# Performance work log

Hardware: AMD Instinct MI355X
Metric: run time of the kernel (lower is better)

## Reference

```python
import jax, jax.numpy as jnp
import numpy as np

B, S, D, H = 2, 2048, 1024, 16
DK = D // H


def setup_inputs() -> dict:
    key = jax.random.key(0)
    ks = jax.random.split(key, 8)
    Q = jax.random.normal(ks[0], (B, S, D), dtype=jnp.float32)
    K = jax.random.normal(ks[1], (B, S, D), dtype=jnp.float32)
    V = jax.random.normal(ks[2], (B, S, D), dtype=jnp.float32)
    scale = 0.02
    W_q = jax.random.normal(ks[3], (D, D), dtype=jnp.float32) * scale
    W_k = jax.random.normal(ks[4], (D, D), dtype=jnp.float32) * scale
    W_v = jax.random.normal(ks[5], (D, D), dtype=jnp.float32) * scale
    W_o = jax.random.normal(ks[6], (D, D), dtype=jnp.float32) * scale
    b_q = jnp.zeros((D,), jnp.float32)
    b_k = jnp.zeros((D,), jnp.float32)
    b_v = jnp.zeros((D,), jnp.float32)
    b_o = jnp.zeros((D,), jnp.float32)
    # causal mask, broadcastable [1,1,S,S]; mask==0 positions are masked out
    mask = jnp.tril(jnp.ones((S, S), jnp.int32))[None, None, :, :]
    return dict(Q=Q, K=K, V=V, W_q=W_q, b_q=b_q, W_k=W_k, b_k=b_k,
                W_v=W_v, b_v=b_v, W_o=W_o, b_o=b_o, mask=mask)


def reference(Q, K, V, W_q, b_q, W_k, b_k, W_v, b_v, W_o, b_o, mask):
    # linear projections (torch Linear equivalent up to weight layout)
    q = Q @ W_q + b_q   # [B,S,D]
    k = K @ W_k + b_k
    v = V @ W_v + b_v
    # split heads -> [B,H,S,DK]
    q = q.reshape(B, S, H, DK).transpose(0, 2, 1, 3)
    k = k.reshape(B, S, H, DK).transpose(0, 2, 1, 3)
    v = v.reshape(B, S, H, DK).transpose(0, 2, 1, 3)
    # scaled dot-product attention with explicit [B,H,S,S] scores
    scores = jnp.einsum('bhqd,bhkd->bhqk', q, k) / jnp.sqrt(jnp.float32(DK))
    scores = jnp.where(mask == 0, jnp.float32(-1e9), scores)
    attn = jax.nn.softmax(scores, axis=-1)
    out = jnp.einsum('bhqk,bhkd->bhqd', attn, v)
    # merge heads and output projection
    out = out.transpose(0, 2, 1, 3).reshape(B, S, D)
    return out @ W_o + b_o
```

## Files before the change

kernel.cpp:

```cpp
#include <hip/hip_runtime.h>


typedef unsigned short u16;
typedef __attribute__((ext_vector_type(8))) short s8v;
typedef __attribute__((ext_vector_type(4))) float f4v;

#define S_ 2048
#define D_ 1024
#define H_ 16
#define DK_ 64

__device__ __forceinline__ u16 f2bf(float f) {
  unsigned u = __builtin_bit_cast(unsigned, f);
  u += 0x7fffu + ((u >> 16) & 1u);
  return (u16)(u >> 16);
}
__device__ __forceinline__ u16 f2bf_t(float f) {
  return (u16)(__builtin_bit_cast(unsigned, f) >> 16);
}

__device__ __forceinline__ void gld_lds16(const u16* g, u16* l) {
  __builtin_amdgcn_global_load_lds(
      (const __attribute__((address_space(1))) unsigned int*)g,
      (__attribute__((address_space(3))) unsigned int*)l, 16, 0, 0);
}

__global__ __launch_bounds__(256) void prep(
    const float* __restrict__ Q, const float* __restrict__ K, const float* __restrict__ V,
    u16* __restrict__ Qc, u16* __restrict__ Kc, u16* __restrict__ Vc,
    const float* __restrict__ W0, const float* __restrict__ W1,
    const float* __restrict__ W2, const float* __restrict__ W3,
    u16* __restrict__ T0, u16* __restrict__ T1, u16* __restrict__ T2, u16* __restrict__ T3) {
  int bid = blockIdx.x, tid = threadIdx.x;
  if (bid < 3072) {
    int z = bid >> 10, t = bid & 1023;
    const float* s = z == 0 ? Q : z == 1 ? K : V;
    u16*         d = z == 0 ? Qc : z == 1 ? Kc : Vc;
    const int n4 = (2 * S_ * D_) / 4;
    for (int idx = t * 256 + tid; idx < n4; idx += 1024 * 256) {
      float4 f = ((const float4*)s)[idx];
      unsigned lo = (unsigned)f2bf(f.x) | ((unsigned)f2bf(f.y) << 16);
      unsigned hi = (unsigned)f2bf(f.z) | ((unsigned)f2bf(f.w) << 16);
      ((uint2*)d)[idx] = make_uint2(lo, hi);
    }
  } else {
    int wb = bid - 3072;
    int z = wb >> 10, t = wb & 1023;
    const float* W = z == 0 ? W0 : z == 1 ? W1 : z == 2 ? W2 : W3;
    u16*         T = z == 0 ? T0 : z == 1 ? T1 : z == 2 ? T2 : T3;
    __shared__ float tile[32][33];
    int tx = tid & 31, ty = tid >> 5;
    int c0 = (t & 31) * 32, r0 = (t >> 5) * 32;
#pragma unroll
    for (int i = 0; i < 32; i += 8)
      tile[ty + i][tx] = W[(size_t)(r0 + ty + i) * D_ + c0 + tx];
    __syncthreads();
#pragma unroll
    for (int i = 0; i < 32; i += 8)
      T[(size_t)(c0 + ty + i) * D_ + r0 + tx] = f2bf(tile[tx][ty + i]);
  }
}

#define BK_ 64

template <int MI, int NJ, int MODE>
__device__ __forceinline__ void gemm_core(const u16* __restrict__ A, const u16* __restrict__ Bt,
                                          const float* __restrict__ bias, void* __restrict__ out,
                                          float oscale, u16* lds) {
  constexpr int BM = MI * 32;
  constexpr int BN = NJ * 32;
  u16* Al = lds;
  u16* Bl = lds + BM * BK_;
  int tid = threadIdx.x;
  int w = tid >> 6, lane = tid & 63, quad = lane >> 4, col = lane & 15;
  int wm = (w >> 1) * (MI * 16), wn = (w & 1) * (NJ * 16);
  int m0 = blockIdx.y * BM, n0 = blockIdx.x * BN;
  f4v acc[MI][NJ] = {};
  const u16* Ag = A + (size_t)m0 * 1024;
  const u16* Bg = Bt + (size_t)n0 * 1024;
  int sr = tid >> 3, ss = tid & 7;

  for (int k0 = 0; k0 < 1024; k0 += BK_) {
    __syncthreads();
#pragma unroll
    for (int c = 0; c < BM / 32; ++c) {
      int r = c * 32 + sr;
      int gs = ss ^ (r & 7);
      gld_lds16(Ag + (size_t)r * 1024 + k0 + gs * 8, &Al[r * BK_ + ss * 8]);
    }
#pragma unroll
    for (int c = 0; c < BN / 32; ++c) {
      int r = c * 32 + sr;
      int gs = ss ^ (r & 7);
      gld_lds16(Bg + (size_t)r * 1024 + k0 + gs * 8, &Bl[r * BK_ + ss * 8]);
    }
    __syncthreads();
#pragma unroll
    for (int hf = 0; hf < 2; ++hf) {
      s8v af[MI], bfr[NJ];
#pragma unroll
      for (int i = 0; i < MI; ++i) {
        int row = wm + i * 16 + col;
        int sl = (hf * 4 + quad) ^ (row & 7);
        af[i] = *(const s8v*)&Al[row * BK_ + sl * 8];
      }
#pragma unroll
      for (int j = 0; j < NJ; ++j) {
        int row = wn + j * 16 + col;
        int sl = (hf * 4 + quad) ^ (row & 7);
        bfr[j] = *(const s8v*)&Bl[row * BK_ + sl * 8];
      }
#pragma unroll
      for (int i = 0; i < MI; ++i)
#pragma unroll
        for (int j = 0; j < NJ; ++j)
          acc[i][j] = __builtin_amdgcn_mfma_f32_16x16x32_bf16(af[i], bfr[j], acc[i][j], 0, 0, 0);
    }
  }

  if (MODE == 1) {
    __syncthreads();
    u16* scr = lds + w * 2304;
    int h = (n0 + wn) >> 6;
    int dkl = lane & 31, sh = (lane >> 5) * 32;
    int mg0 = m0 + wm + sh;
    int bb = mg0 >> 11, s0g = mg0 & 2047;
    u16* ob = (u16*)out + ((size_t)(bb * H_ + h) * DK_) * S_;
#pragma unroll
    for (int t = 0; t < 2; ++t) {
#pragma unroll
      for (int j2 = 2 * t; j2 < 2 * t + 2; ++j2) {
        float bv = bias[n0 + wn + j2 * 16 + col];
        int rloc = j2 * 16 + col - t * 32;
#pragma unroll
        for (int i = 0; i < MI; ++i)
#pragma unroll
          for (int r = 0; r < 4; ++r)
            scr[rloc * 72 + i * 16 + quad * 4 + r] = f2bf(acc[i][j2][r] + bv);
      }
      __builtin_amdgcn_wave_barrier();
      u16* op = ob + (size_t)(t * 32 + dkl) * S_ + s0g;
#pragma unroll
      for (int c = 0; c < 4; ++c)
        *(uint4*)&op[c * 8] = *(const uint4*)&scr[dkl * 72 + sh + c * 8];
      __builtin_amdgcn_wave_barrier();
    }
    return;
  }

#pragma unroll
  for (int i = 0; i < MI; ++i) {
#pragma unroll
    for (int j = 0; j < NJ; ++j) {
      int n = n0 + wn + j * 16 + col;
      float bb = bias[n];
#pragma unroll
      for (int r = 0; r < 4; ++r) {
        int m = m0 + wm + i * 16 + quad * 4 + r;
        float v = (acc[i][j][r] + bb) * oscale;
        if (MODE == 2) {
          ((float*)out)[(size_t)m * 1024 + n] = v;
        } else {
          int b = m >> 11, s = m & 2047, h = n >> 6, dk = n & 63;
          ((u16*)out)[((size_t)(b * H_ + h) * S_ + s) * DK_ + dk] = f2bf(v);
        }
      }
    }
  }
}

#define CEXPQ 0.18033688f

__global__ __launch_bounds__(256) void gemm_qkv(
    const u16* __restrict__ A0, const u16* __restrict__ A1, const u16* __restrict__ A2,
    const u16* __restrict__ B0, const u16* __restrict__ B1, const u16* __restrict__ B2,
    const float* __restrict__ bi0, const float* __restrict__ bi1, const float* __restrict__ bi2,
    u16* __restrict__ o0, u16* __restrict__ o1, u16* __restrict__ o2) {
  __shared__ __attribute__((aligned(16))) u16 lds[128 * BK_ + 128 * BK_];
  int z = blockIdx.z;
  const u16* A = z == 0 ? A0 : z == 1 ? A1 : A2;
  const u16* Bt = z == 0 ? B0 : z == 1 ? B1 : B2;
  const float* bias = z == 0 ? bi0 : z == 1 ? bi1 : bi2;
  u16* o = z == 0 ? o0 : z == 1 ? o1 : o2;
  if (z == 2)
    gemm_core<4, 4, 1>(A, Bt, bias, o, 1.0f, lds);
  else
    gemm_core<4, 4, 0>(A, Bt, bias, o, z == 0 ? CEXPQ : 1.0f, lds);
}

__global__ __launch_bounds__(256, 4) void gemm_out(const u16* __restrict__ A, const u16* __restrict__ Bt,
                                                   const float* __restrict__ bias, float* __restrict__ out) {
  __shared__ __attribute__((aligned(16))) u16 lds[64 * BK_ + 64 * BK_];
  gemm_core<2, 2, 2>(A, Bt, bias, out, 1.0f, lds);
}

#define KT_ 64
#define PSTR 72

__global__ __launch_bounds__(512, 4) void attn_fused(const u16* __restrict__ qb, const u16* __restrict__ kb,
                                                     const u16* __restrict__ vtb, u16* __restrict__ ao) {
  __shared__ __attribute__((aligned(16))) u16 Kt[KT_ * PSTR];
  __shared__ __attribute__((aligned(16))) u16 Vts[DK_ * PSTR];
  __shared__ __attribute__((aligned(16))) u16 Pl[8][16 * PSTR];
  int bh = blockIdx.y, b = bh >> 4, h = bh & 15;
  int j = blockIdx.x;
  int tid = threadIdx.x, w = tid >> 6, lane = tid & 63, quad = lane >> 4, col = lane & 15;
  int sub = w & 3;
  int base = (w < 4) ? (31 - j) * 64 : j * 64;
  int qmin = base + sub * 16;
  int nk = (32 - j) * 64;

  const u16* Qh = qb + (size_t)bh * S_ * DK_;
  const u16* Kh = kb + (size_t)bh * S_ * DK_;
  const u16* Vh = vtb + (size_t)bh * DK_ * S_;

  s8v qf0 = *(const s8v*)(Qh + (size_t)(qmin + col) * DK_ + quad * 8);
  s8v qf1 = *(const s8v*)(Qh + (size_t)(qmin + col) * DK_ + 32 + quad * 8);

  f4v O[4] = {};
  float ls[4] = {};

  int st = tid & 255;
  bool stK = tid < 256;
  int srow = st >> 2, soff = (st & 3) * 16;
  u16* sl = stK ? &Kt[srow * PSTR + soff] : &Vts[srow * PSTR + soff];
  const u16* g0 = stK ? Kh + (size_t)srow * DK_ + soff : Vh + (size_t)srow * S_ + soff;
  uint4 preA = *(const uint4*)g0;
  uint4 preB = *(const uint4*)(g0 + 8);

  for (int kt = 0; kt < nk; kt += KT_) {
    __syncthreads();
    *(uint4*)sl = preA;
    *(uint4*)(sl + 8) = preB;
    __syncthreads();
    int kn = kt + KT_;
    if (kn < nk) {
      const u16* gn = stK ? Kh + (size_t)(kn + srow) * DK_ + soff
                          : Vh + (size_t)srow * S_ + kn + soff;
      preA = *(const uint4*)gn;
      preB = *(const uint4*)(gn + 8);
    }
    if (kt > qmin + 15) continue;

    f4v sc[4];
#pragma unroll
    for (int ks = 0; ks < 4; ++ks) {
      s8v kf0 = *(const s8v*)&Kt[(ks * 16 + col) * PSTR + quad * 8];
      s8v kf1 = *(const s8v*)&Kt[(ks * 16 + col) * PSTR + 32 + quad * 8];
      f4v t = {0.f, 0.f, 0.f, 0.f};
      t = __builtin_amdgcn_mfma_f32_16x16x32_bf16(qf0, kf0, t, 0, 0, 0);
      t = __builtin_amdgcn_mfma_f32_16x16x32_bf16(qf1, kf1, t, 0, 0, 0);
      sc[ks] = t;
    }

    bool full = (kt + KT_ - 1 <= qmin);
#pragma unroll
    for (int r = 0; r < 4; ++r) {
      float p0, p1, p2, p3;
      if (full) {
        p0 = exp2f(sc[0][r]);
        p1 = exp2f(sc[1][r]);
        p2 = exp2f(sc[2][r]);
        p3 = exp2f(sc[3][r]);
      } else {
        int qr = qmin + quad * 4 + r;
        p0 = (kt + col)      <= qr ? exp2f(sc[0][r]) : 0.f;
        p1 = (kt + 16 + col) <= qr ? exp2f(sc[1][r]) : 0.f;
        p2 = (kt + 32 + col) <= qr ? exp2f(sc[2][r]) : 0.f;
        p3 = (kt + 48 + col) <= qr ? exp2f(sc[3][r]) : 0.f;
      }
      ls[r] += (p0 + p1) + (p2 + p3);
      int row = quad * 4 + r;
      Pl[w][row * PSTR + col]      = f2bf_t(p0);
      Pl[w][row * PSTR + 16 + col] = f2bf_t(p1);
      Pl[w][row * PSTR + 32 + col] = f2bf_t(p2);
      Pl[w][row * PSTR + 48 + col] = f2bf_t(p3);
    }
    __builtin_amdgcn_wave_barrier();

    s8v pa0 = *(const s8v*)&Pl[w][col * PSTR + quad * 8];
    s8v pa1 = *(const s8v*)&Pl[w][col * PSTR + 32 + quad * 8];
#pragma unroll
    for (int d = 0; d < 4; ++d) {
      s8v vf0 = *(const s8v*)&Vts[(d * 16 + col) * PSTR + quad * 8];
      s8v vf1 = *(const s8v*)&Vts[(d * 16 + col) * PSTR + 32 + quad * 8];
      O[d] = __builtin_amdgcn_mfma_f32_16x16x32_bf16(pa0, vf0, O[d], 0, 0, 0);
      O[d] = __builtin_amdgcn_mfma_f32_16x16x32_bf16(pa1, vf1, O[d], 0, 0, 0);
    }
    __builtin_amdgcn_wave_barrier();
  }

#pragma unroll
  for (int r = 0; r < 4; ++r) {
    float l = ls[r];
    l += __shfl_xor(l, 1);
    l += __shfl_xor(l, 2);
    l += __shfl_xor(l, 4);
    l += __shfl_xor(l, 8);
    float inv = 1.0f / l;
    size_t row = (size_t)(b * S_ + qmin + quad * 4 + r);
#pragma unroll
    for (int d = 0; d < 4; ++d)
      ao[row * D_ + h * DK_ + d * 16 + col] = f2bf(O[d][r] * inv);
  }
}

extern "C" void kernel_launch(void* const* d_in, const int* in_sizes, int n_in,
                              void* d_out, int out_size, void* d_ws, size_t ws_size,
                              hipStream_t stream) {
  const float* Q  = (const float*)d_in[0];
  const float* K  = (const float*)d_in[1];
  const float* V  = (const float*)d_in[2];
  const float* Wq = (const float*)d_in[3];
  const float* bq = (const float*)d_in[4];
  const float* Wk = (const float*)d_in[5];
  const float* bk = (const float*)d_in[6];
  const float* Wv = (const float*)d_in[7];
  const float* bv = (const float*)d_in[8];
  const float* Wo = (const float*)d_in[9];
  const float* bo = (const float*)d_in[10];

  char* p = (char*)d_ws;
  const size_t TEN = (size_t)2 * S_ * D_ * 2;
  const size_t WT  = (size_t)D_ * D_ * 2;
  u16* Qc  = (u16*)p; p += TEN;
  u16* Kc  = (u16*)p; p += TEN;
  u16* Vc  = (u16*)p; p += TEN;
  u16* Wqt = (u16*)p; p += WT;
  u16* Wkt = (u16*)p; p += WT;
  u16* Wvt = (u16*)p; p += WT;
  u16* Wot = (u16*)p; p += WT;
  u16* qb  = (u16*)p; p += TEN;
  u16* kbf = (u16*)p; p += TEN;
  u16* vtb = (u16*)p; p += TEN;
  u16* ao  = (u16*)p; p += TEN;

  prep<<<7168, 256, 0, stream>>>(Q, K, V, Qc, Kc, Vc, Wq, Wk, Wv, Wo, Wqt, Wkt, Wvt, Wot);
  gemm_qkv<<<dim3(D_ / 128, 32, 3), 256, 0, stream>>>(Qc, Kc, Vc, Wqt, Wkt, Wvt, bq, bk, bv, qb, kbf, vtb);
  attn_fused<<<dim3(16, 2 * H_), 512, 0, stream>>>(qb, kbf, vtb, ao);
  gemm_out<<<dim3(D_ / 64, 64), 256, 0, stream>>>(ao, Wot, bo, (float*)d_out);
}
```

Before: 235.7 us.

## Split attention key range across two blocks and combine partial results

Each attention block now handles only every other 64-key tile (interleaved by a half index), doubling the grid to 1024 blocks. The two blocks write unnormalized bf16 partial outputs and row sums, and a new combine kernel adds them, normalizes, and writes the merged-head layout. This aims to raise occupancy and parallelism on a grid that previously had only 512 blocks. In exchange it adds an extra kernel launch, extra global traffic for the partials, and bf16 rounding of the unnormalized partials. It appears to rely on a fixed softmax offset (no running max), so adding the partials directly is valid.

```diff
diff --git a/kernel.cpp b/kernel.cpp
--- a/kernel.cpp
+++ b/kernel.cpp
@@ -17,6 +17,9 @@
 }
 __device__ __forceinline__ u16 f2bf_t(float f) {
   return (u16)(__builtin_bit_cast(unsigned, f) >> 16);
+}
+__device__ __forceinline__ float bf2f(u16 v) {
+  return __builtin_bit_cast(float, (unsigned)v << 16);
 }
 
 __device__ __forceinline__ void gld_lds16(const u16* g, u16* l) {
@@ -198,12 +201,13 @@
 #define PSTR 72
 
 __global__ __launch_bounds__(512, 4) void attn_fused(const u16* __restrict__ qb, const u16* __restrict__ kb,
-                                                     const u16* __restrict__ vtb, u16* __restrict__ ao) {
+                                                     const u16* __restrict__ vtb,
+                                                     u16* __restrict__ opart, float* __restrict__ lpart) {
   __shared__ __attribute__((aligned(16))) u16 Kt[KT_ * PSTR];
   __shared__ __attribute__((aligned(16))) u16 Vts[DK_ * PSTR];
   __shared__ __attribute__((aligned(16))) u16 Pl[8][16 * PSTR];
-  int bh = blockIdx.y, b = bh >> 4, h = bh & 15;
-  int j = blockIdx.x;
+  int bh = blockIdx.y;
+  int j = blockIdx.x & 15, half = blockIdx.x >> 4;
   int tid = threadIdx.x, w = tid >> 6, lane = tid & 63, quad = lane >> 4, col = lane & 15;
   int sub = w & 3;
   int base = (w < 4) ? (31 - j) * 64 : j * 64;
@@ -213,6 +217,8 @@
   const u16* Qh = qb + (size_t)bh * S_ * DK_;
   const u16* Kh = kb + (size_t)bh * S_ * DK_;
   const u16* Vh = vtb + (size_t)bh * DK_ * S_;
+  u16* Oh = opart + (size_t)half * 32 * S_ * DK_ + (size_t)bh * S_ * DK_;
+  float* Lh = lpart + (size_t)half * 32 * S_ + (size_t)bh * S_;
 
   s8v qf0 = *(const s8v*)(Qh + (size_t)(qmin + col) * DK_ + quad * 8);
   s8v qf1 = *(const s8v*)(Qh + (size_t)(qmin + col) * DK_ + 32 + quad * 8);
@@ -224,16 +230,18 @@
   bool stK = tid < 256;
   int srow = st >> 2, soff = (st & 3) * 16;
   u16* sl = stK ? &Kt[srow * PSTR + soff] : &Vts[srow * PSTR + soff];
-  const u16* g0 = stK ? Kh + (size_t)srow * DK_ + soff : Vh + (size_t)srow * S_ + soff;
+  int kt0 = half * KT_;
+  const u16* g0 = stK ? Kh + (size_t)(kt0 + srow) * DK_ + soff
+                      : Vh + (size_t)srow * S_ + kt0 + soff;
   uint4 preA = *(const uint4*)g0;
   uint4 preB = *(const uint4*)(g0 + 8);
 
-  for (int kt = 0; kt < nk; kt += KT_) {
+  for (int kt = kt0; kt < nk; kt += 2 * KT_) {
     __syncthreads();
     *(uint4*)sl = preA;
     *(uint4*)(sl + 8) = preB;
     __syncthreads();
-    int kn = kt + KT_;
+    int kn = kt + 2 * KT_;
     if (kn < nk) {
       const u16* gn = stK ? Kh + (size_t)(kn + srow) * DK_ + soff
                           : Vh + (size_t)srow * S_ + kn + soff;
@@ -297,12 +305,36 @@
     l += __shfl_xor(l, 2);
     l += __shfl_xor(l, 4);
     l += __shfl_xor(l, 8);
-    float inv = 1.0f / l;
-    size_t row = (size_t)(b * S_ + qmin + quad * 4 + r);
+    int row = qmin + quad * 4 + r;
+    if (col == 0) Lh[row] = l;
 #pragma unroll
     for (int d = 0; d < 4; ++d)
-      ao[row * D_ + h * DK_ + d * 16 + col] = f2bf(O[d][r] * inv);
-  }
+      Oh[(size_t)row * DK_ + d * 16 + col] = f2bf(O[d][r]);
+  }
+}
+
+__global__ __launch_bounds__(256) void attn_combine(const u16* __restrict__ opart,
+                                                    const float* __restrict__ lpart,
+                                                    u16* __restrict__ ao) {
+  int idx = blockIdx.x * 256 + threadIdx.x;
+  int c = idx & 7;
+  int row = idx >> 3;
+  int bh = row >> 11, s = row & 2047;
+  int b = bh >> 4, h = bh & 15;
+  const size_t HALF = (size_t)32 * S_ * DK_;
+  float inv = 1.0f / (lpart[row] + lpart[32 * S_ + row]);
+  uint4 a = *(const uint4*)(opart + (size_t)row * DK_ + c * 8);
+  uint4 bq = *(const uint4*)(opart + HALF + (size_t)row * DK_ + c * 8);
+  const unsigned* au = (const unsigned*)&a;
+  const unsigned* bu = (const unsigned*)&bq;
+  unsigned res[4];
+#pragma unroll
+  for (int i = 0; i < 4; ++i) {
+    float x0 = (bf2f((u16)(au[i] & 0xffff)) + bf2f((u16)(bu[i] & 0xffff))) * inv;
+    float x1 = (bf2f((u16)(au[i] >> 16)) + bf2f((u16)(bu[i] >> 16))) * inv;
+    res[i] = (unsigned)f2bf(x0) | ((unsigned)f2bf(x1) << 16);
+  }
+  *(uint4*)(ao + ((size_t)(b * S_ + s) * D_ + h * DK_ + c * 8)) = *(uint4*)res;
 }
 
 extern "C" void kernel_launch(void* const* d_in, const int* in_sizes, int n_in,
@@ -334,9 +366,12 @@
   u16* kbf = (u16*)p; p += TEN;
   u16* vtb = (u16*)p; p += TEN;
   u16* ao  = (u16*)p; p += TEN;
+  u16* opart = (u16*)p; p += 2 * TEN;
+  float* lpart = (float*)p; p += (size_t)2 * 32 * S_ * 4;
 
   prep<<<7168, 256, 0, stream>>>(Q, K, V, Qc, Kc, Vc, Wq, Wk, Wv, Wo, Wqt, Wkt, Wvt, Wot);
   gemm_qkv<<<dim3(D_ / 128, 32, 3), 256, 0, stream>>>(Qc, Kc, Vc, Wqt, Wkt, Wvt, bq, bk, bv, qb, kbf, vtb);
-  attn_fused<<<dim3(16, 2 * H_), 512, 0, stream>>>(qb, kbf, vtb, ao);
+  attn_fused<<<dim3(32, 2 * H_), 512, 0, stream>>>(qb, kbf, vtb, opart, lpart);
+  attn_combine<<<(32 * S_ * 8) / 256, 256, 0, stream>>>(opart, lpart, ao);
   gemm_out<<<dim3(D_ / 64, 64), 256, 0, stream>>>(ao, Wot, bo, (float*)d_out);
 }
```

New measurement: 242.5 us. 2.9% more time.
